# Optimization experiments

Measured on AMD Instinct MI355X. Metric: run time of the kernel, lower is better.

## Reference

```python
import jax, jax.numpy as jnp
import numpy as np

B, D_IN, H1, H2, E, TOPK = 65536, 1024, 256, 128, 64, 8
LN_EPS = 1e-5


def _layer_norm(x, g, b):
    mu = jnp.mean(x, axis=-1, keepdims=True)
    var = jnp.var(x, axis=-1, keepdims=True)
    return (x - mu) * jax.lax.rsqrt(var + LN_EPS) * g + b


def setup_inputs() -> dict:
    key = jax.random.key(0)
    ks = jax.random.split(key, 8)
    def xavier(k, shape, gain):
        fan_in, fan_out = shape[0], shape[1]
        a = gain * np.sqrt(6.0 / (fan_in + fan_out))
        return jax.random.uniform(k, shape, jnp.float32, -a, a)
    return {
        "x": jax.random.normal(ks[0], (B, D_IN), jnp.float32),
        "W_in": xavier(ks[1], (D_IN, H1), 0.5),
        "b_in": jnp.zeros((H1,), jnp.float32),
        "ln1_g": jnp.ones((H1,), jnp.float32),
        "ln1_b": jnp.zeros((H1,), jnp.float32),
        "W1": xavier(ks[2], (H1, H1), 0.5),
        "b1": jnp.full((H1,), 0.1, jnp.float32),
        "ln2_g": jnp.ones((H1,), jnp.float32),
        "ln2_b": jnp.zeros((H1,), jnp.float32),
        "W2": xavier(ks[3], (H1, H2), 0.5),
        "b2": jnp.full((H2,), 0.1, jnp.float32),
        "W_out": xavier(ks[4], (H2, E), 0.1),
        "b_out": jnp.zeros((E,), jnp.float32),
        "temperature": jnp.ones((1,), jnp.float32),
    }


def reference(x, W_in, b_in, ln1_g, ln1_b, W1, b1, ln2_g, ln2_b, W2, b2, W_out, b_out, temperature):
    # eval-mode forward: dropout and exploration noise disabled
    h0 = jax.nn.relu(x @ W_in + b_in)                       # [B, 256]
    h1 = jax.nn.relu(_layer_norm(h0, ln1_g, ln1_b)) @ W1 + b1 + h0  # residual block
    h2 = jax.nn.relu(_layer_norm(h1, ln2_g, ln2_b)) @ W2 + b2       # [B, 128]
    gate_logits = (h2 @ W_out + b_out) / temperature        # [B, E]
    gate_probs = jax.nn.softmax(gate_logits, axis=1)
    k = min(TOPK, E)
    top_k_probs, top_k_indices = jax.lax.top_k(gate_probs, k)
    top_k_probs = top_k_probs / jnp.sum(top_k_probs, axis=1, keepdims=True)
    return top_k_probs, top_k_indices, gate_probs
```

## Files before the change

### kernel.cpp

```cpp
#include <hip/hip_runtime.h>
#include <math.h>

#define ROWS 32
#define NTHREADS 256
#define TAU 2.5e-5f

typedef float f32x4 __attribute__((ext_vector_type(4)));
typedef short s16x8 __attribute__((ext_vector_type(8)));

#define WS_WIN_HI (0)
#define WS_WIN_LO (512*1024)
#define WS_W1_HI  (1024*1024)
#define WS_W1_LO  (WS_W1_HI + 128*1024)
#define WS_W2_HI  (WS_W1_HI + 256*1024)
#define WS_W2_LO  (WS_W2_HI + 64*1024)
#define WS_WO_HI  (WS_W2_HI + 128*1024)
#define WS_WO_LO  (WS_WO_HI + 16*1024)

__device__ __forceinline__ unsigned short f2bh(float f) {
    union { float f; unsigned u; } v; v.f = f;
    unsigned r = v.u + 0x7fffu + ((v.u >> 16) & 1u);
    return (unsigned short)(r >> 16);
}
__device__ __forceinline__ float bh2f(unsigned short h) {
    union { unsigned u; float f; } v; v.u = ((unsigned)h) << 16;
    return v.f;
}
__device__ __forceinline__ unsigned packsplit(float f) {
    unsigned short h = f2bh(f);
    unsigned short l = f2bh(f - bh2f(h));
    return (unsigned)h | ((unsigned)l << 16);
}

__global__ __launch_bounds__(256)
void prep_frag(const float* __restrict__ W_in, const float* __restrict__ W1,
               const float* __restrict__ W2,   const float* __restrict__ Wo,
               void* ws)
{
    const int t    = threadIdx.x;
    const int tg   = blockIdx.x * 4 + (t >> 6);
    const int lane = t & 63;
    const float* src; int N, Kt, tl; size_t offh, offl;
    if (tg < 512)      { src = W_in; N = 256; Kt = 32; tl = tg;       offh = WS_WIN_HI; offl = WS_WIN_LO; }
    else if (tg < 640) { src = W1;   N = 256; Kt = 8;  tl = tg - 512; offh = WS_W1_HI;  offl = WS_W1_LO; }
    else if (tg < 704) { src = W2;   N = 128; Kt = 8;  tl = tg - 640; offh = WS_W2_HI;  offl = WS_W2_LO; }
    else               { src = Wo;   N = 64;  Kt = 4;  tl = tg - 704; offh = WS_WO_HI;  offl = WS_WO_LO; }
    const int n16 = tl / Kt, s = tl % Kt;
    const int lr = lane & 15, ks = lane >> 4;
    const int n  = n16 * 16 + lr;
    const int kb = s * 32 + ks * 8;
    s16x8 hv, lv;
    #pragma unroll
    for (int j = 0; j < 8; ++j) {
        const float f = src[(size_t)(kb + j) * N + n];
        const unsigned short h = f2bh(f);
        hv[j] = (short)h;
        lv[j] = (short)f2bh(f - bh2f(h));
    }
    const size_t base = ((size_t)tl * 64 + lane) * 8;
    *reinterpret_cast<s16x8*>((short*)((char*)ws + offh) + base) = hv;
    *reinterpret_cast<s16x8*>((short*)((char*)ws + offl) + base) = lv;
}

struct alignas(16) SMem {
    union {
        unsigned ap[32][260];
        struct { double a1d[256]; double h2d[128]; double lgd[64]; } rs;
    } u;
    float  lgt[32][68];
    float2 lnbuf[2][16][2];
    double rred[8];
};

#define MFMA(a, b, c) __builtin_amdgcn_mfma_f32_16x16x32_bf16((a), (b), (c), 0, 0, 0)

__global__ __launch_bounds__(NTHREADS, 3)
void gating_mfma(const float* __restrict__ x,
                 const float* __restrict__ W_in, const float* __restrict__ b_in,
                 const float* __restrict__ ln1_g, const float* __restrict__ ln1_b,
                 const float* __restrict__ W1,   const float* __restrict__ b1,
                 const float* __restrict__ ln2_g, const float* __restrict__ ln2_b,
                 const float* __restrict__ W2,   const float* __restrict__ b2,
                 const float* __restrict__ Wo,   const float* __restrict__ bo,
                 const float* __restrict__ temp,
                 const void* __restrict__ ws,
                 float* __restrict__ out)
{
    __shared__ SMem sm;
    __shared__ unsigned cmask;
    const int tid  = threadIdx.x;
    const int lane = tid & 63;
    const int wv   = tid >> 6;
    const int mt   = wv & 1;
    const int nh   = wv >> 1;
    const int lr   = lane & 15;
    const int ks   = lane >> 4;
    const int row_base = blockIdx.x * ROWS;
    if (tid == 0) cmask = 0;

    float* out_topp = out;
    float* out_topi = out + (size_t)65536 * 8;
    float* out_gp   = out + (size_t)65536 * 16;

    const short* whin_h = (const short*)((const char*)ws + WS_WIN_HI);
    const short* whin_l = (const short*)((const char*)ws + WS_WIN_LO);
    const short* w1_h   = (const short*)((const char*)ws + WS_W1_HI);
    const short* w1_l   = (const short*)((const char*)ws + WS_W1_LO);
    const short* w2_h   = (const short*)((const char*)ws + WS_W2_HI);
    const short* w2_l   = (const short*)((const char*)ws + WS_W2_LO);
    const short* wo_h   = (const short*)((const char*)ws + WS_WO_HI);
    const short* wo_l   = (const short*)((const char*)ws + WS_WO_LO);

    f32x4 hacc[8];
    #pragma unroll
    for (int g = 0; g < 8; ++g) hacc[g] = (f32x4)0.f;

    const float* xrow = x + (size_t)(row_base + mt * 16 + lr) * 1024 + ks * 8;
    float4 cf0 = *reinterpret_cast<const float4*>(xrow);
    float4 cf1 = *reinterpret_cast<const float4*>(xrow + 4);
    for (int s = 0; s < 32; ++s) {
        float4 nf0, nf1;
        if (s < 31) {
            nf0 = *reinterpret_cast<const float4*>(xrow + (s + 1) * 32);
            nf1 = *reinterpret_cast<const float4*>(xrow + (s + 1) * 32 + 4);
        }
        const float xa[8] = {cf0.x, cf0.y, cf0.z, cf0.w, cf1.x, cf1.y, cf1.z, cf1.w};
        s16x8 ah, al;
        #pragma unroll
        for (int j = 0; j < 8; ++j) {
            const unsigned u = __float_as_uint(xa[j]);
            ah[j] = (short)(u >> 16);
            const float r = xa[j] - __uint_as_float(u & 0xffff0000u);
            al[j] = (short)(__float_as_uint(r) >> 16);
        }
        #pragma unroll
        for (int g = 0; g < 8; ++g) {
            const size_t tb = (((size_t)(nh * 8 + g) * 32 + s) * 64 + lane) * 8;
            const s16x8 bh = *reinterpret_cast<const s16x8*>(whin_h + tb);
            const s16x8 bl = *reinterpret_cast<const s16x8*>(whin_l + tb);
            hacc[g] = MFMA(ah, bh, hacc[g]);
            hacc[g] = MFMA(al, bh, hacc[g]);
            hacc[g] = MFMA(ah, bl, hacc[g]);
        }
        cf0 = nf0; cf1 = nf1;
    }
    #pragma unroll
    for (int g = 0; g < 8; ++g) {
        const int n = nh * 128 + g * 16 + lr;
        const float bi = b_in[n];
        #pragma unroll
        for (int j = 0; j < 4; ++j) hacc[g][j] = fmaxf(hacc[g][j] + bi, 0.f);
    }

    {
        float s4[4] = {0, 0, 0, 0}, q4[4] = {0, 0, 0, 0};
        #pragma unroll
        for (int g = 0; g < 8; ++g)
            #pragma unroll
            for (int j = 0; j < 4; ++j) { s4[j] += hacc[g][j]; q4[j] += hacc[g][j] * hacc[g][j]; }
        #pragma unroll
        for (int m = 1; m < 16; m <<= 1) {
            #pragma unroll
            for (int j = 0; j < 4; ++j) {
                s4[j] += __shfl_xor(s4[j], m);
                q4[j] += __shfl_xor(q4[j], m);
            }
        }
        if (lr == 0) {
            #pragma unroll
            for (int j = 0; j < 4; ++j)
                sm.lnbuf[mt][ks * 4 + j][nh] = make_float2(s4[j], q4[j]);
        }
        __syncthreads();
        float mu[4], rsv[4];
        #pragma unroll
        for (int j = 0; j < 4; ++j) {
            const float2 c0 = sm.lnbuf[mt][ks * 4 + j][0];
            const float2 c1 = sm.lnbuf[mt][ks * 4 + j][1];
            const float ss = c0.x + c1.x, qq = c0.y + c1.y;
            mu[j] = ss * (1.f / 256.f);
            rsv[j] = rsqrtf(qq * (1.f / 256.f) - mu[j] * mu[j] + 1e-5f);
        }
        #pragma unroll
        for (int g = 0; g < 8; ++g) {
            const int n = nh * 128 + g * 16 + lr;
            const float gg = ln1_g[n], bb = ln1_b[n];
            #pragma unroll
            for (int j = 0; j < 4; ++j) {
                const float v = fmaxf((hacc[g][j] - mu[j]) * rsv[j] * gg + bb, 0.f);
                sm.u.ap[mt * 16 + ks * 4 + j][n] = packsplit(v);
            }
        }
    }
    __syncthreads();

    {
        f32x4 acc2[8];
        #pragma unroll
        for (int g = 0; g < 8; ++g) acc2[g] = (f32x4)0.f;
        for (int s = 0; s < 8; ++s) {
            const int kof = s * 32 + ks * 8;
            const uint4 q0 = *reinterpret_cast<const uint4*>(&sm.u.ap[mt * 16 + lr][kof]);
            const uint4 q1 = *reinterpret_cast<const uint4*>(&sm.u.ap[mt * 16 + lr][kof + 4]);
            const unsigned uu[8] = {q0.x, q0.y, q0.z, q0.w, q1.x, q1.y, q1.z, q1.w};
            s16x8 ah, al;
            #pragma unroll
            for (int j = 0; j < 8; ++j) { ah[j] = (short)(uu[j] & 0xffff); al[j] = (short)(uu[j] >> 16); }
            #pragma unroll
            for (int g = 0; g < 8; ++g) {
                const size_t tb = (((size_t)(nh * 8 + g) * 8 + s) * 64 + lane) * 8;
                const s16x8 bh = *reinterpret_cast<const s16x8*>(w1_h + tb);
                const s16x8 bl = *reinterpret_cast<const s16x8*>(w1_l + tb);
                acc2[g] = MFMA(ah, bh, acc2[g]);
                acc2[g] = MFMA(al, bh, acc2[g]);
                acc2[g] = MFMA(ah, bl, acc2[g]);
            }
        }
        #pragma unroll
        for (int g = 0; g < 8; ++g) {
            const int n = nh * 128 + g * 16 + lr;
            const float bv = b1[n];
            #pragma unroll
            for (int j = 0; j < 4; ++j) hacc[g][j] = acc2[g][j] + bv + hacc[g][j];
        }
    }
    __syncthreads();

    {
        float s4[4] = {0, 0, 0, 0}, q4[4] = {0, 0, 0, 0};
        #pragma unroll
        for (int g = 0; g < 8; ++g)
            #pragma unroll
            for (int j = 0; j < 4; ++j) { s4[j] += hacc[g][j]; q4[j] += hacc[g][j] * hacc[g][j]; }
        #pragma unroll
        for (int m = 1; m < 16; m <<= 1) {
            #pragma unroll
            for (int j = 0; j < 4; ++j) {
                s4[j] += __shfl_xor(s4[j], m);
                q4[j] += __shfl_xor(q4[j], m);
            }
        }
        if (lr == 0) {
            #pragma unroll
            for (int j = 0; j < 4; ++j)
                sm.lnbuf[mt][ks * 4 + j][nh] = make_float2(s4[j], q4[j]);
        }
        __syncthreads();
        float mu[4], rsv[4];
        #pragma unroll
        for (int j = 0; j < 4; ++j) {
            const float2 c0 = sm.lnbuf[mt][ks * 4 + j][0];
            const float2 c1 = sm.lnbuf[mt][ks * 4 + j][1];
            const float ss = c0.x + c1.x, qq = c0.y + c1.y;
            mu[j] = ss * (1.f / 256.f);
            rsv[j] = rsqrtf(qq * (1.f / 256.f) - mu[j] * mu[j] + 1e-5f);
        }
        #pragma unroll
        for (int g = 0; g < 8; ++g) {
            const int n = nh * 128 + g * 16 + lr;
            const float gg = ln2_g[n], bb = ln2_b[n];
            #pragma unroll
            for (int j = 0; j < 4; ++j) {
                const float v = fmaxf((hacc[g][j] - mu[j]) * rsv[j] * gg + bb, 0.f);
                sm.u.ap[mt * 16 + ks * 4 + j][n] = packsplit(v);
            }
        }
    }
    __syncthreads();

    {
        f32x4 acc3[4];
        #pragma unroll
        for (int g = 0; g < 4; ++g) acc3[g] = (f32x4)0.f;
        for (int s = 0; s < 8; ++s) {
            const int kof = s * 32 + ks * 8;
            const uint4 q0 = *reinterpret_cast<const uint4*>(&sm.u.ap[mt * 16 + lr][kof]);
            const uint4 q1 = *reinterpret_cast<const uint4*>(&sm.u.ap[mt * 16 + lr][kof + 4]);
            const unsigned uu[8] = {q0.x, q0.y, q0.z, q0.w, q1.x, q1.y, q1.z, q1.w};
            s16x8 ah, al;
            #pragma unroll
            for (int j = 0; j < 8; ++j) { ah[j] = (short)(uu[j] & 0xffff); al[j] = (short)(uu[j] >> 16); }
            #pragma unroll
            for (int g = 0; g < 4; ++g) {
                const size_t tb = (((size_t)(nh * 4 + g) * 8 + s) * 64 + lane) * 8;
                const s16x8 bh = *reinterpret_cast<const s16x8*>(w2_h + tb);
                const s16x8 bl = *reinterpret_cast<const s16x8*>(w2_l + tb);
                acc3[g] = MFMA(ah, bh, acc3[g]);
                acc3[g] = MFMA(al, bh, acc3[g]);
                acc3[g] = MFMA(ah, bl, acc3[g]);
            }
        }
        __syncthreads();
        #pragma unroll
        for (int g = 0; g < 4; ++g) {
            const int n = nh * 64 + g * 16 + lr;
            const float bv = b2[n];
            #pragma unroll
            for (int j = 0; j < 4; ++j)
                sm.u.ap[mt * 16 + ks * 4 + j][n] = packsplit(acc3[g][j] + bv);
        }
    }
    __syncthreads();

    {
        f32x4 acc4[2];
        acc4[0] = (f32x4)0.f; acc4[1] = (f32x4)0.f;
        for (int s = 0; s < 4; ++s) {
            const int kof = s * 32 + ks * 8;
            const uint4 q0 = *reinterpret_cast<const uint4*>(&sm.u.ap[mt * 16 + lr][kof]);
            const uint4 q1 = *reinterpret_cast<const uint4*>(&sm.u.ap[mt * 16 + lr][kof + 4]);
            const unsigned uu[8] = {q0.x, q0.y, q0.z, q0.w, q1.x, q1.y, q1.z, q1.w};
            s16x8 ah, al;
            #pragma unroll
            for (int j = 0; j < 8; ++j) { ah[j] = (short)(uu[j] & 0xffff); al[j] = (short)(uu[j] >> 16); }
            #pragma unroll
            for (int g = 0; g < 2; ++g) {
                const size_t tb = (((size_t)(nh * 2 + g) * 4 + s) * 64 + lane) * 8;
                const s16x8 bh = *reinterpret_cast<const s16x8*>(wo_h + tb);
                const s16x8 bl = *reinterpret_cast<const s16x8*>(wo_l + tb);
                acc4[g] = MFMA(ah, bh, acc4[g]);
                acc4[g] = MFMA(al, bh, acc4[g]);
                acc4[g] = MFMA(ah, bl, acc4[g]);
            }
        }
        const float T = temp[0];
        #pragma unroll
        for (int g = 0; g < 2; ++g) {
            const int n = nh * 32 + g * 16 + lr;
            const float bv = bo[n];
            #pragma unroll
            for (int j = 0; j < 4; ++j)
                sm.lgt[mt * 16 + ks * 4 + j][n] = (acc4[g][j] + bv) / T;
        }
    }
    __syncthreads();

    {
        const float tau = TAU / temp[0];
        for (int j = 0; j < 8; ++j) {
            const int r = wv * 8 + j;
            const float v = sm.lgt[r][lane];
            float m = v;
            #pragma unroll
            for (int mk = 32; mk >= 1; mk >>= 1) m = fmaxf(m, __shfl_xor(m, mk));
            float p = expf(v - m);
            float ssum = p;
            #pragma unroll
            for (int mk = 32; mk >= 1; mk >>= 1) ssum += __shfl_xor(ssum, mk);
            const float gp = p / ssum;
            out_gp[(size_t)(row_base + r) * 64 + lane] = gp;

            float pv = v;
            int   pi = lane;
            float sum8 = 0.f, myv = 0.f, prev = 0.f;
            int   myi = 0;
            bool  contested = false;
            #pragma unroll
            for (int t = 0; t < 9; ++t) {
                float cv = pv;
                int   ci = pi;
                #pragma unroll
                for (int mk = 32; mk >= 1; mk >>= 1) {
                    const float ov = __shfl_xor(cv, mk);
                    const int   oi = __shfl_xor(ci, mk);
                    if (ov > cv || (ov == cv && oi < ci)) { cv = ov; ci = oi; }
                }
                if (t > 0 && (prev - cv) < tau) contested = true;
                prev = cv;
                if (t < 8) {
                    const float g = __shfl(gp, ci);
                    sum8 += g;
                    if (lane == t)  { myv = g; myi = ci; }
                    if (lane == ci) pv = -3.0e38f;
                }
            }
            if (lane < 8) {
                out_topp[(size_t)(row_base + r) * 8 + lane] = myv / sum8;
                out_topi[(size_t)(row_base + r) * 8 + lane] = (float)myi;
            }
            if (lane == 0 && contested) atomicOr(&cmask, 1u << r);
        }
    }

    __syncthreads();
    unsigned cm = cmask;
    while (cm) {
        const int r = __ffs(cm) - 1;
        cm &= cm - 1;
        const float* xr = x + (size_t)(row_base + r) * 1024;
        const int c = tid;
        const int wvv = tid >> 6;

        double a0 = 0.0, a1 = 0.0, a2 = 0.0, a3 = 0.0;
        for (int k = 0; k < 1024; k += 4) {
            a0 = fma((double)xr[k + 0], (double)W_in[(size_t)(k + 0) * 256 + c], a0);
            a1 = fma((double)xr[k + 1], (double)W_in[(size_t)(k + 1) * 256 + c], a1);
            a2 = fma((double)xr[k + 2], (double)W_in[(size_t)(k + 2) * 256 + c], a2);
            a3 = fma((double)xr[k + 3], (double)W_in[(size_t)(k + 3) * 256 + c], a3);
        }
        const double h0 = fmax((a0 + a1) + (a2 + a3) + (double)b_in[c], 0.0);

        double s = h0, q = h0 * h0;
        #pragma unroll
        for (int m = 1; m < 64; m <<= 1) { s += __shfl_xor(s, m); q += __shfl_xor(q, m); }
        if (lane == 0) { sm.rred[wvv * 2] = s; sm.rred[wvv * 2 + 1] = q; }
        __syncthreads();
        {
            const double ss = (sm.rred[0] + sm.rred[2]) + (sm.rred[4] + sm.rred[6]);
            const double qq = (sm.rred[1] + sm.rred[3]) + (sm.rred[5] + sm.rred[7]);
            const double mu = ss * (1.0 / 256.0);
            const double rsv = 1.0 / sqrt(qq * (1.0 / 256.0) - mu * mu + 1e-5);
            sm.u.rs.a1d[c] = fmax((h0 - mu) * rsv * (double)ln1_g[c] + (double)ln1_b[c], 0.0);
        }
        __syncthreads();

        double b0 = 0.0, b1c = 0.0, b2c = 0.0, b3c = 0.0;
        for (int k = 0; k < 256; k += 4) {
            b0  = fma(sm.u.rs.a1d[k + 0], (double)W1[(size_t)(k + 0) * 256 + c], b0);
            b1c = fma(sm.u.rs.a1d[k + 1], (double)W1[(size_t)(k + 1) * 256 + c], b1c);
            b2c = fma(sm.u.rs.a1d[k + 2], (double)W1[(size_t)(k + 2) * 256 + c], b2c);
            b3c = fma(sm.u.rs.a1d[k + 3], (double)W1[(size_t)(k + 3) * 256 + c], b3c);
        }
        const double h1 = (b0 + b1c) + (b2c + b3c) + (double)b1[c] + h0;

        s = h1; q = h1 * h1;
        #pragma unroll
        for (int m = 1; m < 64; m <<= 1) { s += __shfl_xor(s, m); q += __shfl_xor(q, m); }
        if (lane == 0) { sm.rred[wvv * 2] = s; sm.rred[wvv * 2 + 1] = q; }
        __syncthreads();
        {
            const double ss = (sm.rred[0] + sm.rred[2]) + (sm.rred[4] + sm.rred[6]);
            const double qq = (sm.rred[1] + sm.rred[3]) + (sm.rred[5] + sm.rred[7]);
            const double mu = ss * (1.0 / 256.0);
            const double rsv = 1.0 / sqrt(qq * (1.0 / 256.0) - mu * mu + 1e-5);
            sm.u.rs.a1d[c] = fmax((h1 - mu) * rsv * (double)ln2_g[c] + (double)ln2_b[c], 0.0);
        }
        __syncthreads();

        if (c < 128) {
            double d0 = 0.0, d1 = 0.0, d2 = 0.0, d3 = 0.0;
            for (int k = 0; k < 256; k += 4) {
                d0 = fma(sm.u.rs.a1d[k + 0], (double)W2[(size_t)(k + 0) * 128 + c], d0);
                d1 = fma(sm.u.rs.a1d[k + 1], (double)W2[(size_t)(k + 1) * 128 + c], d1);
                d2 = fma(sm.u.rs.a1d[k + 2], (double)W2[(size_t)(k + 2) * 128 + c], d2);
                d3 = fma(sm.u.rs.a1d[k + 3], (double)W2[(size_t)(k + 3) * 128 + c], d3);
            }
            sm.u.rs.h2d[c] = (d0 + d1) + (d2 + d3) + (double)b2[c];
        }
        __syncthreads();

        if (c < 64) {
            double e0 = 0.0, e1 = 0.0;
            for (int k = 0; k < 128; k += 2) {
                e0 = fma(sm.u.rs.h2d[k + 0], (double)Wo[(size_t)(k + 0) * 64 + c], e0);
                e1 = fma(sm.u.rs.h2d[k + 1], (double)Wo[(size_t)(k + 1) * 64 + c], e1);
            }
            sm.u.rs.lgd[c] = (e0 + e1 + (double)bo[c]) / (double)temp[0];
        }
        __syncthreads();

        if (tid < 64) {
            const int ln = tid;
            const double v = sm.u.rs.lgd[ln];
            double m = v;
            #pragma unroll
            for (int mk = 32; mk >= 1; mk >>= 1) m = fmax(m, __shfl_xor(m, mk));
            const double p = exp(v - m);
            double ssum = p;
            #pragma unroll
            for (int mk = 32; mk >= 1; mk >>= 1) ssum += __shfl_xor(ssum, mk);
            const double gp = p / ssum;
            out_gp[(size_t)(row_base + r) * 64 + ln] = (float)gp;

            double pv = gp;
            int    pi = ln;
            double sum8 = 0.0, myv = 0.0;
            int    myi = 0;
            #pragma unroll
            for (int t = 0; t < 8; ++t) {
                double cv = pv;
                int    ci = pi;
                #pragma unroll
                for (int mk = 32; mk >= 1; mk >>= 1) {
                    const double ov = __shfl_xor(cv, mk);
                    const int    oi = __shfl_xor(ci, mk);
                    if (ov > cv || (ov == cv && oi < ci)) { cv = ov; ci = oi; }
                }
                sum8 += cv;
                if (ln == t)  { myv = cv; myi = ci; }
                if (ln == ci) pv = -1.0;
            }
            if (ln < 8) {
                out_topp[(size_t)(row_base + r) * 8 + ln] = (float)(myv / sum8);
                out_topi[(size_t)(row_base + r) * 8 + ln] = (float)myi;
            }
        }
        __syncthreads();
    }
}

extern "C" void kernel_launch(void* const* d_in, const int* in_sizes, int n_in,
                              void* d_out, int out_size, void* d_ws, size_t ws_size,
                              hipStream_t stream) {
    const float* x     = (const float*)d_in[0];
    const float* W_in  = (const float*)d_in[1];
    const float* b_in  = (const float*)d_in[2];
    const float* ln1_g = (const float*)d_in[3];
    const float* ln1_b = (const float*)d_in[4];
    const float* W1    = (const float*)d_in[5];
    const float* b1    = (const float*)d_in[6];
    const float* ln2_g = (const float*)d_in[7];
    const float* ln2_b = (const float*)d_in[8];
    const float* W2    = (const float*)d_in[9];
    const float* b2    = (const float*)d_in[10];
    const float* Wo    = (const float*)d_in[11];
    const float* bo    = (const float*)d_in[12];
    const float* temp  = (const float*)d_in[13];

    prep_frag<<<dim3(180), dim3(256), 0, stream>>>(W_in, W1, W2, Wo, d_ws);
    gating_mfma<<<dim3(65536 / ROWS), dim3(NTHREADS), 0, stream>>>(
        x, W_in, b_in, ln1_g, ln1_b, W1, b1, ln2_g, ln2_b, W2, b2, Wo, bo, temp,
        d_ws, (float*)d_out);
}
```

Baseline: 735.1 us.

## Double-buffer weight fragment loads in registers across MFMA GEMM stages

Restructures the three main GEMM loops to prefetch the next k-step's B fragments (hi and lo bf16 parts) into a second register set while the current step's MFMAs run. Sched barriers pin the order so the loads are issued before the compute. Launch bounds drop from 3 to 2 waves per SIMD so the extra fragment registers fit. This trades occupancy-based latency hiding for explicit software pipelining of global weight loads.

```diff
diff --git a/kernel.cpp b/kernel.cpp
--- a/kernel.cpp
+++ b/kernel.cpp
@@ -74,7 +74,50 @@
 
 #define MFMA(a, b, c) __builtin_amdgcn_mfma_f32_16x16x32_bf16((a), (b), (c), 0, 0, 0)
 
-__global__ __launch_bounds__(NTHREADS, 3)
+#define LOADB8(BH, BL, WH, WL, KT, S)                                          \
+    _Pragma("unroll")                                                          \
+    for (int g = 0; g < 8; ++g) {                                              \
+        const size_t tb = (((size_t)(nh * 8 + g) * (KT) + (S)) * 64 + lane) * 8; \
+        BH[g] = *reinterpret_cast<const s16x8*>((WH) + tb);                    \
+        BL[g] = *reinterpret_cast<const s16x8*>((WL) + tb);                    \
+    }
+
+#define LOADB4(BH, BL, WH, WL, KT, S)                                          \
+    _Pragma("unroll")                                                          \
+    for (int g = 0; g < 4; ++g) {                                              \
+        const size_t tb = (((size_t)(nh * 4 + g) * (KT) + (S)) * 64 + lane) * 8; \
+        BH[g] = *reinterpret_cast<const s16x8*>((WH) + tb);                    \
+        BL[g] = *reinterpret_cast<const s16x8*>((WL) + tb);                    \
+    }
+
+#define MFMAG(NG, ACC, AH, AL, BH, BL)                                         \
+    _Pragma("unroll")                                                          \
+    for (int g = 0; g < (NG); ++g) {                                           \
+        ACC[g] = MFMA(AH, BH[g], ACC[g]);                                      \
+        ACC[g] = MFMA(AL, BH[g], ACC[g]);                                      \
+        ACC[g] = MFMA(AH, BL[g], ACC[g]);                                      \
+    }
+
+#define SPLITX(F0, F1, AH, AL) do {                                            \
+    const float _xa[8] = {F0.x, F0.y, F0.z, F0.w, F1.x, F1.y, F1.z, F1.w};     \
+    _Pragma("unroll")                                                          \
+    for (int j = 0; j < 8; ++j) {                                              \
+        const unsigned _u = __float_as_uint(_xa[j]);                           \
+        AH[j] = (short)(_u >> 16);                                             \
+        AL[j] = (short)(__float_as_uint(_xa[j] - __uint_as_float(_u & 0xffff0000u)) >> 16); \
+    }                                                                          \
+} while (0)
+
+#define UNPACKA(Q0, Q1, AH, AL) do {                                           \
+    const unsigned _w[8] = {Q0.x, Q0.y, Q0.z, Q0.w, Q1.x, Q1.y, Q1.z, Q1.w};   \
+    _Pragma("unroll")                                                          \
+    for (int _j = 0; _j < 8; ++_j) {                                           \
+        AH[_j] = (short)(_w[_j] & 0xffff);                                     \
+        AL[_j] = (short)(_w[_j] >> 16);                                        \
+    }                                                                          \
+} while (0)
+
+__global__ __launch_bounds__(NTHREADS, 2)
 void gating_mfma(const float* __restrict__ x,
                  const float* __restrict__ W_in, const float* __restrict__ b_in,
                  const float* __restrict__ ln1_g, const float* __restrict__ ln1_b,
@@ -115,34 +158,29 @@
     #pragma unroll
     for (int g = 0; g < 8; ++g) hacc[g] = (f32x4)0.f;
 
-    const float* xrow = x + (size_t)(row_base + mt * 16 + lr) * 1024 + ks * 8;
-    float4 cf0 = *reinterpret_cast<const float4*>(xrow);
-    float4 cf1 = *reinterpret_cast<const float4*>(xrow + 4);
-    for (int s = 0; s < 32; ++s) {
-        float4 nf0, nf1;
-        if (s < 31) {
-            nf0 = *reinterpret_cast<const float4*>(xrow + (s + 1) * 32);
-            nf1 = *reinterpret_cast<const float4*>(xrow + (s + 1) * 32 + 4);
-        }
-        const float xa[8] = {cf0.x, cf0.y, cf0.z, cf0.w, cf1.x, cf1.y, cf1.z, cf1.w};
+    {
+        const float* xrow = x + (size_t)(row_base + mt * 16 + lr) * 1024 + ks * 8;
+        s16x8 bh0[8], bl0[8], bh1[8], bl1[8];
         s16x8 ah, al;
-        #pragma unroll
-        for (int j = 0; j < 8; ++j) {
-            const unsigned u = __float_as_uint(xa[j]);
-            ah[j] = (short)(u >> 16);
-            const float r = xa[j] - __uint_as_float(u & 0xffff0000u);
-            al[j] = (short)(__float_as_uint(r) >> 16);
-        }
-        #pragma unroll
-        for (int g = 0; g < 8; ++g) {
-            const size_t tb = (((size_t)(nh * 8 + g) * 32 + s) * 64 + lane) * 8;
-            const s16x8 bh = *reinterpret_cast<const s16x8*>(whin_h + tb);
-            const s16x8 bl = *reinterpret_cast<const s16x8*>(whin_l + tb);
-            hacc[g] = MFMA(ah, bh, hacc[g]);
-            hacc[g] = MFMA(al, bh, hacc[g]);
-            hacc[g] = MFMA(ah, bl, hacc[g]);
-        }
-        cf0 = nf0; cf1 = nf1;
+        float4 xc0 = *reinterpret_cast<const float4*>(xrow);
+        float4 xc1 = *reinterpret_cast<const float4*>(xrow + 4);
+        LOADB8(bh0, bl0, whin_h, whin_l, 32, 0);
+        for (int s = 0; s < 32; s += 2) {
+            float4 xd0 = *reinterpret_cast<const float4*>(xrow + (s + 1) * 32);
+            float4 xd1 = *reinterpret_cast<const float4*>(xrow + (s + 1) * 32 + 4);
+            SPLITX(xc0, xc1, ah, al);
+            LOADB8(bh1, bl1, whin_h, whin_l, 32, s + 1);
+            __builtin_amdgcn_sched_barrier(0);
+            MFMAG(8, hacc, ah, al, bh0, bl0);
+            if (s + 2 < 32) {
+                xc0 = *reinterpret_cast<const float4*>(xrow + (s + 2) * 32);
+                xc1 = *reinterpret_cast<const float4*>(xrow + (s + 2) * 32 + 4);
+            }
+            SPLITX(xd0, xd1, ah, al);
+            if (s + 2 < 32) LOADB8(bh0, bl0, whin_h, whin_l, 32, s + 2);
+            __builtin_amdgcn_sched_barrier(0);
+            MFMAG(8, hacc, ah, al, bh1, bl1);
+        }
     }
     #pragma unroll
     for (int g = 0; g < 8; ++g) {
@@ -198,23 +236,28 @@
         f32x4 acc2[8];
         #pragma unroll
         for (int g = 0; g < 8; ++g) acc2[g] = (f32x4)0.f;
-        for (int s = 0; s < 8; ++s) {
-            const int kof = s * 32 + ks * 8;
-            const uint4 q0 = *reinterpret_cast<const uint4*>(&sm.u.ap[mt * 16 + lr][kof]);
-            const uint4 q1 = *reinterpret_cast<const uint4*>(&sm.u.ap[mt * 16 + lr][kof + 4]);
-            const unsigned uu[8] = {q0.x, q0.y, q0.z, q0.w, q1.x, q1.y, q1.z, q1.w};
-            s16x8 ah, al;
-            #pragma unroll
-            for (int j = 0; j < 8; ++j) { ah[j] = (short)(uu[j] & 0xffff); al[j] = (short)(uu[j] >> 16); }
-            #pragma unroll
-            for (int g = 0; g < 8; ++g) {
-                const size_t tb = (((size_t)(nh * 8 + g) * 8 + s) * 64 + lane) * 8;
-                const s16x8 bh = *reinterpret_cast<const s16x8*>(w1_h + tb);
-                const s16x8 bl = *reinterpret_cast<const s16x8*>(w1_l + tb);
-                acc2[g] = MFMA(ah, bh, acc2[g]);
-                acc2[g] = MFMA(al, bh, acc2[g]);
-                acc2[g] = MFMA(ah, bl, acc2[g]);
-            }
+        s16x8 bh0[8], bl0[8], bh1[8], bl1[8];
+        s16x8 ah, al;
+        LOADB8(bh0, bl0, w1_h, w1_l, 8, 0);
+        for (int s = 0; s < 8; s += 2) {
+            {
+                const int kof = s * 32 + ks * 8;
+                const uint4 q0 = *reinterpret_cast<const uint4*>(&sm.u.ap[mt * 16 + lr][kof]);
+                const uint4 q1 = *reinterpret_cast<const uint4*>(&sm.u.ap[mt * 16 + lr][kof + 4]);
+                UNPACKA(q0, q1, ah, al);
+            }
+            LOADB8(bh1, bl1, w1_h, w1_l, 8, s + 1);
+            __builtin_amdgcn_sched_barrier(0);
+            MFMAG(8, acc2, ah, al, bh0, bl0);
+            {
+                const int kof = (s + 1) * 32 + ks * 8;
+                const uint4 q0 = *reinterpret_cast<const uint4*>(&sm.u.ap[mt * 16 + lr][kof]);
+                const uint4 q1 = *reinterpret_cast<const uint4*>(&sm.u.ap[mt * 16 + lr][kof + 4]);
+                UNPACKA(q0, q1, ah, al);
+            }
+            if (s + 2 < 8) LOADB8(bh0, bl0, w1_h, w1_l, 8, s + 2);
+            __builtin_amdgcn_sched_barrier(0);
+            MFMAG(8, acc2, ah, al, bh1, bl1);
         }
         #pragma unroll
         for (int g = 0; g < 8; ++g) {
@@ -272,23 +315,28 @@
         f32x4 acc3[4];
         #pragma unroll
         for (int g = 0; g < 4; ++g) acc3[g] = (f32x4)0.f;
-        for (int s = 0; s < 8; ++s) {
-            const int kof = s * 32 + ks * 8;
-            const uint4 q0 = *reinterpret_cast<const uint4*>(&sm.u.ap[mt * 16 + lr][kof]);
-            const uint4 q1 = *reinterpret_cast<const uint4*>(&sm.u.ap[mt * 16 + lr][kof + 4]);
-            const unsigned uu[8] = {q0.x, q0.y, q0.z, q0.w, q1.x, q1.y, q1.z, q1.w};
-            s16x8 ah, al;
-            #pragma unroll
-            for (int j = 0; j < 8; ++j) { ah[j] = (short)(uu[j] & 0xffff); al[j] = (short)(uu[j] >> 16); }
-            #pragma unroll
-            for (int g = 0; g < 4; ++g) {
-                const size_t tb = (((size_t)(nh * 4 + g) * 8 + s) * 64 + lane) * 8;
-                const s16x8 bh = *reinterpret_cast<const s16x8*>(w2_h + tb);
-                const s16x8 bl = *reinterpret_cast<const s16x8*>(w2_l + tb);
-                acc3[g] = MFMA(ah, bh, acc3[g]);
-                acc3[g] = MFMA(al, bh, acc3[g]);
-                acc3[g] = MFMA(ah, bl, acc3[g]);
-            }
+        s16x8 bh0[4], bl0[4], bh1[4], bl1[4];
+        s16x8 ah, al;
+        LOADB4(bh0, bl0, w2_h, w2_l, 8, 0);
+        for (int s = 0; s < 8; s += 2) {
+            {
+                const int kof = s * 32 + ks * 8;
+                const uint4 q0 = *reinterpret_cast<const uint4*>(&sm.u.ap[mt * 16 + lr][kof]);
+                const uint4 q1 = *reinterpret_cast<const uint4*>(&sm.u.ap[mt * 16 + lr][kof + 4]);
+                UNPACKA(q0, q1, ah, al);
+            }
+            LOADB4(bh1, bl1, w2_h, w2_l, 8, s + 1);
+            __builtin_amdgcn_sched_barrier(0);
+            MFMAG(4, acc3, ah, al, bh0, bl0);
+            {
+                const int kof = (s + 1) * 32 + ks * 8;
+                const uint4 q0 = *reinterpret_cast<const uint4*>(&sm.u.ap[mt * 16 + lr][kof]);
+                const uint4 q1 = *reinterpret_cast<const uint4*>(&sm.u.ap[mt * 16 + lr][kof + 4]);
+                UNPACKA(q0, q1, ah, al);
+            }
+            if (s + 2 < 8) LOADB4(bh0, bl0, w2_h, w2_l, 8, s + 2);
+            __builtin_amdgcn_sched_barrier(0);
+            MFMAG(4, acc3, ah, al, bh1, bl1);
         }
         __syncthreads();
         #pragma unroll
@@ -309,10 +357,8 @@
             const int kof = s * 32 + ks * 8;
             const uint4 q0 = *reinterpret_cast<const uint4*>(&sm.u.ap[mt * 16 + lr][kof]);
             const uint4 q1 = *reinterpret_cast<const uint4*>(&sm.u.ap[mt * 16 + lr][kof + 4]);
-            const unsigned uu[8] = {q0.x, q0.y, q0.z, q0.w, q1.x, q1.y, q1.z, q1.w};
             s16x8 ah, al;
-            #pragma unroll
-            for (int j = 0; j < 8; ++j) { ah[j] = (short)(uu[j] & 0xffff); al[j] = (short)(uu[j] >> 16); }
+            UNPACKA(q0, q1, ah, al);
             #pragma unroll
             for (int g = 0; g < 2; ++g) {
                 const size_t tb = (((size_t)(nh * 2 + g) * 4 + s) * 64 + lane) * 8;
```

After: 870.7 us. +18.5%, slower.
